# Kernel tuning notes

Hardware: AMD Instinct MI355X
Metric: run time of the kernel (lower is better)

Reference implementation:

```python
import jax, jax.numpy as jnp
import numpy as np

N_HEADS = 16


def setup_inputs() -> dict:
    key = jax.random.key(0)
    ks = jax.random.split(key, 9)
    B, S, D = 2, 2048, 1024
    s = 0.02
    return {
        "x": jax.random.normal(ks[0], (B, S, D), dtype=jnp.float32),
        "Wq": jax.random.normal(ks[1], (D, D), dtype=jnp.float32) * s,
        "bq": jax.random.normal(ks[2], (D,), dtype=jnp.float32) * s,
        "Wk": jax.random.normal(ks[3], (D, D), dtype=jnp.float32) * s,
        "bk": jax.random.normal(ks[4], (D,), dtype=jnp.float32) * s,
        "Wv": jax.random.normal(ks[5], (D, D), dtype=jnp.float32) * s,
        "bv": jax.random.normal(ks[6], (D,), dtype=jnp.float32) * s,
        "Wo": jax.random.normal(ks[7], (D, D), dtype=jnp.float32) * s,
        "bo": jax.random.normal(ks[8], (D,), dtype=jnp.float32) * s,
    }


def reference(x, Wq, bq, Wk, bk, Wv, bv, Wo, bo):
    B, S, D = x.shape
    H = N_HEADS
    hd = D // H
    # projections -> [B, H, S, hd]
    def heads(w, b):
        return (x @ w + b).reshape(B, S, H, hd).transpose(0, 2, 1, 3)
    Q, K, V = heads(Wq, bq), heads(Wk, bk), heads(Wv, bv)
    scores = jnp.einsum("bhqd,bhkd->bhqk", Q, K)
    causal = jnp.triu(jnp.ones((S, S), dtype=bool), k=1)  # True above diagonal
    scores = jnp.where(causal, -jnp.inf, scores)
    w = jax.nn.softmax(scores / jnp.sqrt(jnp.float32(hd)), axis=-1)
    ctx = jnp.einsum("bhqk,bhkd->bhqd", w, V).transpose(0, 2, 1, 3).reshape(B, S, D)
    return ctx @ Wo + bo
```

## Files before the change

kernel.cpp:

```cpp
#include <hip/hip_runtime.h>
#include <hip/hip_bf16.h>

typedef __attribute__((ext_vector_type(8))) short short8;
typedef __attribute__((ext_vector_type(4))) float floatx4;
typedef __attribute__((ext_vector_type(4))) int intx4;

#define D_MODEL 1024
#define SEQ     2048
#define NB      2
#define NH      16
#define HD      64
#define MROWS   4096
#define CZ      (0.125f * 1.44269504f)

__device__ __forceinline__ floatx4 mfma_bf16(short8 a, short8 b, floatx4 c) {
  return __builtin_amdgcn_mfma_f32_16x16x32_bf16(a, b, c, 0, 0, 0);
}

__device__ __forceinline__ void dma16(const __hip_bfloat16* g, __hip_bfloat16* l) {
  __builtin_amdgcn_global_load_lds(
      (const __attribute__((address_space(1))) void*)g,
      (__attribute__((address_space(3))) void*)l, 16, 0, 0);
}
#define WAIT_VM(n)  __asm__ __volatile__("s_waitcnt vmcnt(" #n ")" ::: "memory")
#define BARRIER()   __asm__ __volatile__("s_barrier" ::: "memory")

__device__ __forceinline__ int packbf(float a, float b) {
  union { __hip_bfloat16 h; unsigned short u; } x, y;
  x.h = __float2bfloat16(a); y.h = __float2bfloat16(b);
  return (int)(((unsigned)y.u << 16) | (unsigned)x.u);
}

__global__ void convert_x_kernel(const float* __restrict__ x, __hip_bfloat16* __restrict__ xb) {
  int i = (blockIdx.x * 256 + threadIdx.x) * 4;
  float4 v = *(const float4*)(x + i);
  __hip_bfloat16 tmp[4];
  tmp[0] = __float2bfloat16(v.x);
  tmp[1] = __float2bfloat16(v.y);
  tmp[2] = __float2bfloat16(v.z);
  tmp[3] = __float2bfloat16(v.w);
  *(ushort4*)(xb + i) = *(ushort4*)tmp;
}

__global__ void transpose_w_kernel(const float* __restrict__ W0, const float* __restrict__ W1,
                                   const float* __restrict__ W2, const float* __restrict__ W3,
                                   __hip_bfloat16* __restrict__ T0, __hip_bfloat16* __restrict__ T1,
                                   __hip_bfloat16* __restrict__ T2, __hip_bfloat16* __restrict__ T3) {
  const int z = blockIdx.z;
  const float* W = (z == 0) ? W0 : (z == 1) ? W1 : (z == 2) ? W2 : W3;
  __hip_bfloat16* Wt = (z == 0) ? T0 : (z == 1) ? T1 : (z == 2) ? T2 : T3;
  __shared__ float tile[32][33];
  int k0 = blockIdx.x * 32, n0 = blockIdx.y * 32;
  int tx = threadIdx.x, ty = threadIdx.y;
#pragma unroll
  for (int i = 0; i < 4; i++)
    tile[ty + 8 * i][tx] = W[(size_t)(k0 + ty + 8 * i) * D_MODEL + n0 + tx];
  __syncthreads();
#pragma unroll
  for (int i = 0; i < 4; i++)
    Wt[(size_t)(n0 + ty + 8 * i) * D_MODEL + k0 + tx] = __float2bfloat16(tile[tx][ty + 8 * i]);
}

template <int MODE>
__global__ __launch_bounds__(256) void gemm_kernel(
    const __hip_bfloat16* __restrict__ X,
    const __hip_bfloat16* __restrict__ Wt0, const __hip_bfloat16* __restrict__ Wt1,
    const __hip_bfloat16* __restrict__ Wt2,
    const float* __restrict__ b0, const float* __restrict__ b1, const float* __restrict__ b2,
    void* __restrict__ out0, void* __restrict__ out1, void* __restrict__ out2) {
  constexpr int MT = (MODE == 0) ? 128 : 64;
  constexpr int I = MT / 32;
  constexpr int NKT = D_MODEL / 32;

  const int z = blockIdx.y;
  const __hip_bfloat16* Wt = (z == 0) ? Wt0 : (z == 1) ? Wt1 : Wt2;
  const float* bias = (z == 0) ? b0 : (z == 1) ? b1 : b2;
  void* outp = (z == 0) ? out0 : (z == 1) ? out1 : out2;
  const float scale = (MODE == 0 && z == 0) ? CZ : 1.f;

  __shared__ __attribute__((aligned(16))) __hip_bfloat16 As[3][MT * 32];
  __shared__ __attribute__((aligned(16))) __hip_bfloat16 Bs[3][128 * 32];

  const int n0 = blockIdx.x * 128;
  const int m0 = blockIdx.z * MT;
  const int t = threadIdx.x;
  const int lane = t & 63, w = t >> 6;
  const int wm = (w >> 1) * (MT / 2), wn = (w & 1) * 64;
  const int lr = lane & 15;
  const int lq = lane >> 4;

  const __hip_bfloat16* Xp = X + (size_t)m0 * D_MODEL;
  const __hip_bfloat16* Wp = Wt + (size_t)n0 * D_MODEL;

  const int lrow = lane >> 2;
  const int skg = (lane & 3) << 3;
  const int srowA = ((MT == 128) ? (w << 5) : (w << 4)) + lrow;
  const int sbA0 = (((MT == 128) ? (w << 5) : (w << 4)) << 5);
  const int sbA1 = sbA0 + (16 << 5);
  const int srowB = (w << 5) + lrow;
  const int sbB0 = ((w << 5) << 5);
  const int sbB1 = sbB0 + (16 << 5);

#define STAGE_G(kt_, buf_)                                                              \
  {                                                                                     \
    const int kn_ = (kt_) * 32;                                                         \
    dma16(Xp + (size_t)srowA * D_MODEL + kn_ + skg, &As[buf_][sbA0]);                   \
    if (MT == 128) dma16(Xp + (size_t)(srowA + 16) * D_MODEL + kn_ + skg, &As[buf_][sbA1]); \
    dma16(Wp + (size_t)srowB * D_MODEL + kn_ + skg, &Bs[buf_][sbB0]);                   \
    dma16(Wp + (size_t)(srowB + 16) * D_MODEL + kn_ + skg, &Bs[buf_][sbB1]);            \
  }

  floatx4 acc[I][4];
#pragma unroll
  for (int i = 0; i < I; i++)
#pragma unroll
    for (int j = 0; j < 4; j++) acc[i][j] = (floatx4){0.f, 0.f, 0.f, 0.f};

  STAGE_G(0, 0);
  STAGE_G(1, 1);

  int cb = 0;
  for (int kt = 0; kt < NKT; kt++) {
    if (kt < NKT - 1) {
      if constexpr (MODE == 0) WAIT_VM(4);
      else                     WAIT_VM(3);
    } else {
      WAIT_VM(0);
    }
    BARRIER();
    if (kt + 2 < NKT) {
      const int nb = (cb == 0) ? 2 : cb - 1;
      STAGE_G(kt + 2, nb);
    }
    const __hip_bfloat16* Ac = As[cb];
    const __hip_bfloat16* Bc = Bs[cb];
    short8 af[I], bfr[4];
#pragma unroll
    for (int i = 0; i < I; i++) af[i] = *(const short8*)&Ac[(wm + i * 16 + lr) * 32 + lq * 8];
#pragma unroll
    for (int j = 0; j < 4; j++) bfr[j] = *(const short8*)&Bc[(wn + j * 16 + lr) * 32 + lq * 8];
#pragma unroll
    for (int i = 0; i < I; i++)
#pragma unroll
      for (int j = 0; j < 4; j++) acc[i][j] = mfma_bf16(af[i], bfr[j], acc[i][j]);
    cb = (cb == 2) ? 0 : cb + 1;
  }
#undef STAGE_G

#pragma unroll
  for (int j = 0; j < 4; j++) {
    const int n = n0 + wn + j * 16 + lr;
    const float bv = bias[n];
#pragma unroll
    for (int i = 0; i < I; i++) {
      const int mb = m0 + wm + i * 16 + lq * 4;
      if (MODE == 0) {
        __hip_bfloat16* O = (__hip_bfloat16*)outp;
        const int b = mb >> 11, s = mb & 2047;
        const int h = n >> 6, d = n & 63;
        if (z == 2) {
          ushort4 pk;
          __hip_bfloat16* pp = (__hip_bfloat16*)&pk;
#pragma unroll
          for (int r = 0; r < 4; r++) pp[r] = __float2bfloat16(acc[i][j][r] + bv);
          *(ushort4*)(O + (((size_t)(b * NH + h) * HD + d) * SEQ + s)) = pk;
        } else {
#pragma unroll
          for (int r = 0; r < 4; r++)
            O[(((size_t)(b * NH + h) * SEQ + (s + r)) * HD) + d] =
                __float2bfloat16((acc[i][j][r] + bv) * scale);
        }
      } else {
#pragma unroll
        for (int r = 0; r < 4; r++)
          ((float*)outp)[(size_t)(mb + r) * D_MODEL + n] = acc[i][j][r] + bv;
      }
    }
  }
}

__global__ __launch_bounds__(512, 4) void attn_kernel(
    const __hip_bfloat16* __restrict__ Q, const __hip_bfloat16* __restrict__ Kg,
    const __hip_bfloat16* __restrict__ Vt, __hip_bfloat16* __restrict__ ctx) {
  const int bh = blockIdx.x;
  const int b = bh >> 4, h = bh & 15;
  const int p = blockIdx.y;
  const int t = threadIdx.x, lane = t & 63, w = t >> 6;
  const int lr = lane & 15, lq = lane >> 4;
  const int wr = w & 3, wb = w >> 2;

  __shared__ __attribute__((aligned(16))) __hip_bfloat16 Ks[2][128 * 64];
  __shared__ __attribute__((aligned(16))) __hip_bfloat16 VTs[2][64 * 128];

  const __hip_bfloat16* Qb = Q + (size_t)bh * SEQ * HD;
  const __hip_bfloat16* Kb = Kg + (size_t)bh * SEQ * HD;
  const __hip_bfloat16* Vb = Vt + (size_t)bh * HD * SEQ;

  short8 qf[2][2];
#pragma unroll
  for (int ph = 0; ph < 2; ph++) {
    const int qt = ph ? 31 - p : p;
    const int rw = qt * 64 + wr * 16;
#pragma unroll
    for (int ks = 0; ks < 2; ks++)
      qf[ph][ks] = *(const short8*)(Qb + (size_t)(rw + lr) * HD + ks * 32 + lq * 8);
  }

  const int kr0 = (w << 4) + (lane >> 3);
  const int kg0 = (lane & 7) ^ (kr0 & 7);
  const int kr1 = kr0 + 8;
  const int kg1 = (lane & 7) ^ (kr1 & 7);
  const int kb0 = (w << 4) << 6;
  const int kb1 = ((w << 4) + 8) << 6;
  const int vr0 = (w << 3) + (lane >> 4);
  const int vg0 = (lane & 15) ^ (vr0 & 15);
  const int vr1 = vr0 + 4;
  const int vg1 = (lane & 15) ^ (vr1 & 15);
  const int vb0 = (w << 3) << 7;
  const int vb1 = ((w << 3) + 4) << 7;

  const int nktA = (p + 2) >> 1;
  const int TOT = 17;

#define STAGE(nn, nb)                                                           \
  {                                                                             \
    dma16(Kb + ((size_t)((nn) + kr0) << 6) + (kg0 << 3), &Ks[nb][kb0]);         \
    dma16(Kb + ((size_t)((nn) + kr1) << 6) + (kg1 << 3), &Ks[nb][kb1]);         \
    dma16(Vb + (size_t)vr0 * SEQ + (nn) + (vg0 << 3), &VTs[nb][vb0]);           \
    dma16(Vb + (size_t)vr1 * SEQ + (nn) + (vg1 << 3), &VTs[nb][vb1]);           \
  }

  STAGE(0, 0);
  int g = 0;

  const int idx0 = (lr + ((lq & 1) << 5)) << 2;
  const int idx1 = idx0 + 64;
  const bool hi = (lq >= 2);

  for (int ph = 0; ph < 2; ph++) {
    const int qt = ph ? 31 - p : p;
    const int nkt = (qt + 2) >> 1;
    const int rw = qt * 64 + wr * 16;
    const int q = rw + lr;

    floatx4 o[4];
#pragma unroll
    for (int dt = 0; dt < 4; dt++) o[dt] = (floatx4){0.f, 0.f, 0.f, 0.f};
    float ls = 0.f;

    for (int kt = 0; kt < nkt; kt++, g++) {
      WAIT_VM(0);
      BARRIER();
      if (g + 1 < TOT) {
        const int gn = g + 1;
        const int ktn = (gn < nktA) ? gn : gn - nktA;
        STAGE(ktn << 7, gn & 1);
      }
      const int n0 = (kt << 7) + (wb << 6);
      if (n0 <= rw + 15) {
        const __hip_bfloat16* Kc = Ks[g & 1];
        const __hip_bfloat16* Vc = VTs[g & 1];

        floatx4 s[4];
#pragma unroll
        for (int nt = 0; nt < 4; nt++) s[nt] = (floatx4){0.f, 0.f, 0.f, 0.f};
#pragma unroll
        for (int ks = 0; ks < 2; ks++) {
#pragma unroll
          for (int nt = 0; nt < 4; nt++) {
            const int row = (wb << 6) + (nt << 4) + lr;
            short8 kf = *(const short8*)&Kc[(row << 6) + ((((ks << 2) + lq) ^ (row & 7)) << 3)];
            s[nt] = mfma_bf16(kf, qf[ph][ks], s[nt]);
          }
        }

        int pkA[4], pkB[4];
        if (n0 + 63 > rw) {
#pragma unroll
          for (int nt = 0; nt < 4; nt++) {
            const int kbase = n0 + (nt << 4) + (lq << 2);
            float pe[4];
#pragma unroll
            for (int r = 0; r < 4; r++) {
              pe[r] = (kbase + r <= q) ? exp2f(s[nt][r]) : 0.f;
              ls += pe[r];
            }
            pkA[nt] = packbf(pe[0], pe[1]);
            pkB[nt] = packbf(pe[2], pe[3]);
          }
        } else {
#pragma unroll
          for (int nt = 0; nt < 4; nt++) {
            float pe[4];
#pragma unroll
            for (int r = 0; r < 4; r++) {
              pe[r] = exp2f(s[nt][r]);
              ls += pe[r];
            }
            pkA[nt] = packbf(pe[0], pe[1]);
            pkB[nt] = packbf(pe[2], pe[3]);
          }
        }

#pragma unroll
        for (int ks = 0; ks < 2; ks++) {
          const int t0 = 2 * ks, t1 = 2 * ks + 1;
          int c0a = __builtin_amdgcn_ds_bpermute(idx0, pkA[t0]);
          int c0b = __builtin_amdgcn_ds_bpermute(idx0, pkA[t1]);
          int c1a = __builtin_amdgcn_ds_bpermute(idx0, pkB[t0]);
          int c1b = __builtin_amdgcn_ds_bpermute(idx0, pkB[t1]);
          int c2a = __builtin_amdgcn_ds_bpermute(idx1, pkA[t0]);
          int c2b = __builtin_amdgcn_ds_bpermute(idx1, pkA[t1]);
          int c3a = __builtin_amdgcn_ds_bpermute(idx1, pkB[t0]);
          int c3b = __builtin_amdgcn_ds_bpermute(idx1, pkB[t1]);
          intx4 bi;
          bi[0] = hi ? c0b : c0a;
          bi[1] = hi ? c1b : c1a;
          bi[2] = hi ? c2b : c2a;
          bi[3] = hi ? c3b : c3a;
          short8 pf = __builtin_bit_cast(short8, bi);
#pragma unroll
          for (int dt = 0; dt < 4; dt++) {
            const int row = (dt << 4) + lr;
            const int gv = (wb << 3) + (ks << 2) + lq;
            short8 vf = *(const short8*)&Vc[(row << 7) + ((gv ^ (row & 15)) << 3)];
            o[dt] = mfma_bf16(vf, pf, o[dt]);
          }
        }
      }
    }

    const int fb = (g - 1) & 1;
    BARRIER();
    {
      float* od = (float*)&Ks[fb][0];
      float* ld = (float*)&VTs[fb][0];
      const int base = (wr << 10) + (lane << 4);
      if (wb == 1) {
#pragma unroll
        for (int dt = 0; dt < 4; dt++) *(floatx4*)&od[base + (dt << 2)] = o[dt];
        ld[(wr << 6) + lane] = ls;
      }
      BARRIER();
      if (wb == 0) {
#pragma unroll
        for (int dt = 0; dt < 4; dt++) o[dt] += *(const floatx4*)&od[base + (dt << 2)];
        ls += ld[(wr << 6) + lane];
        ls += __shfl_xor(ls, 16);
        ls += __shfl_xor(ls, 32);
        const float inv = 1.f / ls;
        __hip_bfloat16* cp = ctx + (size_t)b * SEQ * D_MODEL + h * HD + (size_t)q * D_MODEL;
#pragma unroll
        for (int dt = 0; dt < 4; dt++) {
          ushort4 pk;
          __hip_bfloat16* pp = (__hip_bfloat16*)&pk;
#pragma unroll
          for (int r = 0; r < 4; r++) pp[r] = __float2bfloat16(o[dt][r] * inv);
          *(ushort4*)(cp + (dt << 4) + (lq << 2)) = pk;
        }
      }
    }
  }
#undef STAGE
}

extern "C" void kernel_launch(void* const* d_in, const int* in_sizes, int n_in,
                              void* d_out, int out_size, void* d_ws, size_t ws_size,
                              hipStream_t stream) {
  const float* x  = (const float*)d_in[0];
  const float* Wq = (const float*)d_in[1];
  const float* bq = (const float*)d_in[2];
  const float* Wk = (const float*)d_in[3];
  const float* bk = (const float*)d_in[4];
  const float* Wv = (const float*)d_in[5];
  const float* bv = (const float*)d_in[6];
  const float* Wo = (const float*)d_in[7];
  const float* bo = (const float*)d_in[8];

  char* ws = (char*)d_ws;
  const size_t MB = 1u << 20;
  __hip_bfloat16* xb  = (__hip_bfloat16*)(ws + 0 * MB);
  __hip_bfloat16* wtq = (__hip_bfloat16*)(ws + 8 * MB);
  __hip_bfloat16* wtk = (__hip_bfloat16*)(ws + 10 * MB);
  __hip_bfloat16* wtv = (__hip_bfloat16*)(ws + 12 * MB);
  __hip_bfloat16* wto = (__hip_bfloat16*)(ws + 14 * MB);
  __hip_bfloat16* qb  = (__hip_bfloat16*)(ws + 16 * MB);
  __hip_bfloat16* kb  = (__hip_bfloat16*)(ws + 24 * MB);
  __hip_bfloat16* vt  = (__hip_bfloat16*)(ws + 32 * MB);
  __hip_bfloat16* ctx = xb;

  convert_x_kernel<<<4096, 256, 0, stream>>>(x, xb);
  transpose_w_kernel<<<dim3(32, 32, 4), dim3(32, 8), 0, stream>>>(Wq, Wk, Wv, Wo,
                                                                  wtq, wtk, wtv, wto);
  gemm_kernel<0><<<dim3(8, 3, 32), 256, 0, stream>>>(xb, wtq, wtk, wtv, bq, bk, bv,
                                                     (void*)qb, (void*)kb, (void*)vt);
  attn_kernel<<<dim3(32, 16), 512, 0, stream>>>(qb, kb, vt, ctx);
  gemm_kernel<1><<<dim3(8, 1, 64), 256, 0, stream>>>(ctx, wto, wto, wto, bo, bo, bo,
                                                     d_out, d_out, d_out);
}
```

Measured before the change: 199.8 us.

## Halve attention block to 4 waves with two row tiles each; fuse prep kernels

The attention kernel drops from 8 to 4 waves per block. Each wave now computes two 16-row query tiles, so every K and V fragment read from LDS is reused across two MFMAs. Masked scores are set to a large negative before exp, bf16 packing uses a perm-based round instead of the library conversion, and the cross-wave reduction gets its own LDS buffers. The x conversion and weight transpose launches are merged into one prep kernel to save a launch. In exchange, register pressure rises and there are fewer waves per CU to hide latency.

```diff
diff --git a/kernel.cpp b/kernel.cpp
--- a/kernel.cpp
+++ b/kernel.cpp
@@ -24,29 +24,35 @@
 }
 #define WAIT_VM(n)  __asm__ __volatile__("s_waitcnt vmcnt(" #n ")" ::: "memory")
 #define BARRIER()   __asm__ __volatile__("s_barrier" ::: "memory")
-
-__device__ __forceinline__ int packbf(float a, float b) {
-  union { __hip_bfloat16 h; unsigned short u; } x, y;
-  x.h = __float2bfloat16(a); y.h = __float2bfloat16(b);
-  return (int)(((unsigned)y.u << 16) | (unsigned)x.u);
-}
-
-__global__ void convert_x_kernel(const float* __restrict__ x, __hip_bfloat16* __restrict__ xb) {
-  int i = (blockIdx.x * 256 + threadIdx.x) * 4;
-  float4 v = *(const float4*)(x + i);
-  __hip_bfloat16 tmp[4];
-  tmp[0] = __float2bfloat16(v.x);
-  tmp[1] = __float2bfloat16(v.y);
-  tmp[2] = __float2bfloat16(v.z);
-  tmp[3] = __float2bfloat16(v.w);
-  *(ushort4*)(xb + i) = *(ushort4*)tmp;
-}
-
-__global__ void transpose_w_kernel(const float* __restrict__ W0, const float* __restrict__ W1,
-                                   const float* __restrict__ W2, const float* __restrict__ W3,
-                                   __hip_bfloat16* __restrict__ T0, __hip_bfloat16* __restrict__ T1,
-                                   __hip_bfloat16* __restrict__ T2, __hip_bfloat16* __restrict__ T3) {
+#define WAIT_LGKM() __asm__ __volatile__("s_waitcnt lgkmcnt(0)" ::: "memory")
+
+__device__ __forceinline__ int pack2bf(float a, float b) {
+  unsigned ua = __builtin_bit_cast(unsigned, a) + 0x8000u;
+  unsigned ub = __builtin_bit_cast(unsigned, b) + 0x8000u;
+  return (int)__builtin_amdgcn_perm(ub, ua, 0x07060302u);
+}
+
+__global__ void prep_kernel(const float* __restrict__ x, __hip_bfloat16* __restrict__ xb,
+                            const float* __restrict__ W0, const float* __restrict__ W1,
+                            const float* __restrict__ W2, const float* __restrict__ W3,
+                            __hip_bfloat16* __restrict__ T0, __hip_bfloat16* __restrict__ T1,
+                            __hip_bfloat16* __restrict__ T2, __hip_bfloat16* __restrict__ T3) {
   const int z = blockIdx.z;
+  if (z == 4) {
+    const int tid = threadIdx.y * 32 + threadIdx.x;
+    const int base = ((blockIdx.y * 32 + blockIdx.x) * 256 + tid) * 16;
+#pragma unroll
+    for (int c = 0; c < 4; c++) {
+      float4 v = *(const float4*)(x + base + c * 4);
+      __hip_bfloat16 tmp[4];
+      tmp[0] = __float2bfloat16(v.x);
+      tmp[1] = __float2bfloat16(v.y);
+      tmp[2] = __float2bfloat16(v.z);
+      tmp[3] = __float2bfloat16(v.w);
+      *(ushort4*)(xb + base + c * 4) = *(ushort4*)tmp;
+    }
+    return;
+  }
   const float* W = (z == 0) ? W0 : (z == 1) ? W1 : (z == 2) ? W2 : W3;
   __hip_bfloat16* Wt = (z == 0) ? T0 : (z == 1) ? T1 : (z == 2) ? T2 : T3;
   __shared__ float tile[32][33];
@@ -179,7 +185,7 @@
   }
 }
 
-__global__ __launch_bounds__(512, 4) void attn_kernel(
+__global__ __launch_bounds__(256, 2) void attn_kernel(
     const __hip_bfloat16* __restrict__ Q, const __hip_bfloat16* __restrict__ Kg,
     const __hip_bfloat16* __restrict__ Vt, __hip_bfloat16* __restrict__ ctx) {
   const int bh = blockIdx.x;
@@ -187,48 +193,51 @@
   const int p = blockIdx.y;
   const int t = threadIdx.x, lane = t & 63, w = t >> 6;
   const int lr = lane & 15, lq = lane >> 4;
-  const int wr = w & 3, wb = w >> 2;
+  const int wr = w & 1, wb = w >> 1;
 
   __shared__ __attribute__((aligned(16))) __hip_bfloat16 Ks[2][128 * 64];
   __shared__ __attribute__((aligned(16))) __hip_bfloat16 VTs[2][64 * 128];
+  __shared__ __attribute__((aligned(16))) float dumpO[2048];
+  __shared__ float dumpL[256];
 
   const __hip_bfloat16* Qb = Q + (size_t)bh * SEQ * HD;
   const __hip_bfloat16* Kb = Kg + (size_t)bh * SEQ * HD;
   const __hip_bfloat16* Vb = Vt + (size_t)bh * HD * SEQ;
 
-  short8 qf[2][2];
+  short8 qf[2][2][2];
 #pragma unroll
   for (int ph = 0; ph < 2; ph++) {
     const int qt = ph ? 31 - p : p;
-    const int rw = qt * 64 + wr * 16;
-#pragma unroll
-    for (int ks = 0; ks < 2; ks++)
-      qf[ph][ks] = *(const short8*)(Qb + (size_t)(rw + lr) * HD + ks * 32 + lq * 8);
-  }
-
-  const int kr0 = (w << 4) + (lane >> 3);
-  const int kg0 = (lane & 7) ^ (kr0 & 7);
-  const int kr1 = kr0 + 8;
-  const int kg1 = (lane & 7) ^ (kr1 & 7);
-  const int kb0 = (w << 4) << 6;
-  const int kb1 = ((w << 4) + 8) << 6;
-  const int vr0 = (w << 3) + (lane >> 4);
-  const int vg0 = (lane & 15) ^ (vr0 & 15);
-  const int vr1 = vr0 + 4;
-  const int vg1 = (lane & 15) ^ (vr1 & 15);
-  const int vb0 = (w << 3) << 7;
-  const int vb1 = ((w << 3) + 4) << 7;
+#pragma unroll
+    for (int rt = 0; rt < 2; rt++)
+#pragma unroll
+      for (int ks = 0; ks < 2; ks++)
+        qf[ph][rt][ks] = *(const short8*)(Qb + (size_t)(qt * 64 + wr * 32 + rt * 16 + lr) * HD +
+                                          ks * 32 + lq * 8);
+  }
+
+  const int krow = (w << 5) + (lane >> 3);
+  const int ksl = lane & 7;
+  const int vrow = (w << 4) + (lane >> 4);
+  const int vsl = lane & 15;
+
+#define STAGE(tb, nb)                                                                     \
+  {                                                                                       \
+    _Pragma("unroll") for (int i = 0; i < 4; i++) {                                       \
+      const int r_ = krow + i * 8;                                                        \
+      dma16(Kb + ((size_t)((tb) + r_) << 6) + ((ksl ^ (r_ & 7)) << 3),                    \
+            &Ks[nb][((w << 5) + i * 8) << 6]);                                            \
+    }                                                                                     \
+    _Pragma("unroll") for (int i = 0; i < 4; i++) {                                       \
+      const int r_ = vrow + i * 4;                                                        \
+      dma16(Vb + (size_t)r_ * SEQ + (tb) + ((vsl ^ (r_ & 15)) << 3),                      \
+            &VTs[nb][((w << 4) + i * 4) << 7]);                                           \
+    }                                                                                     \
+  }
 
   const int nktA = (p + 2) >> 1;
   const int TOT = 17;
-
-#define STAGE(nn, nb)                                                           \
-  {                                                                             \
-    dma16(Kb + ((size_t)((nn) + kr0) << 6) + (kg0 << 3), &Ks[nb][kb0]);         \
-    dma16(Kb + ((size_t)((nn) + kr1) << 6) + (kg1 << 3), &Ks[nb][kb1]);         \
-    dma16(Vb + (size_t)vr0 * SEQ + (nn) + (vg0 << 3), &VTs[nb][vb0]);           \
-    dma16(Vb + (size_t)vr1 * SEQ + (nn) + (vg1 << 3), &VTs[nb][vb1]);           \
-  }
+#define KTN(gs) (((gs) < nktA) ? (gs) : (gs)-nktA)
 
   STAGE(0, 0);
   int g = 0;
@@ -237,131 +246,163 @@
   const int idx1 = idx0 + 64;
   const bool hi = (lq >= 2);
 
+  const int kfb0 = (lr << 6) + ((lq ^ (lr & 7)) << 3);
+  const int kfb1 = (lr << 6) + (((4 + lq) ^ (lr & 7)) << 3);
+  const int vfb0 = (lr << 7) + ((((wb << 3) + lq) ^ lr) << 3);
+  const int vfb1 = (lr << 7) + ((((wb << 3) + 4 + lq) ^ lr) << 3);
+  const int kwoff = wb << 12;
+
   for (int ph = 0; ph < 2; ph++) {
     const int qt = ph ? 31 - p : p;
     const int nkt = (qt + 2) >> 1;
-    const int rw = qt * 64 + wr * 16;
-    const int q = rw + lr;
-
-    floatx4 o[4];
-#pragma unroll
-    for (int dt = 0; dt < 4; dt++) o[dt] = (floatx4){0.f, 0.f, 0.f, 0.f};
-    float ls = 0.f;
+    const int qbase = qt * 64 + wr * 32;
+    const int qmaxw = qbase + 31;
+
+    floatx4 o[2][4];
+#pragma unroll
+    for (int rt = 0; rt < 2; rt++)
+#pragma unroll
+      for (int dt = 0; dt < 4; dt++) o[rt][dt] = (floatx4){0.f, 0.f, 0.f, 0.f};
+    float ls[2] = {0.f, 0.f};
 
     for (int kt = 0; kt < nkt; kt++, g++) {
       WAIT_VM(0);
       BARRIER();
-      if (g + 1 < TOT) {
-        const int gn = g + 1;
-        const int ktn = (gn < nktA) ? gn : gn - nktA;
-        STAGE(ktn << 7, gn & 1);
-      }
-      const int n0 = (kt << 7) + (wb << 6);
-      if (n0 <= rw + 15) {
-        const __hip_bfloat16* Kc = Ks[g & 1];
-        const __hip_bfloat16* Vc = VTs[g & 1];
-
-        floatx4 s[4];
-#pragma unroll
-        for (int nt = 0; nt < 4; nt++) s[nt] = (floatx4){0.f, 0.f, 0.f, 0.f};
-#pragma unroll
-        for (int ks = 0; ks < 2; ks++) {
+      if (g + 1 < TOT) STAGE(KTN(g + 1) << 7, (g + 1) & 1);
+
+      const int n0w = (kt << 7) + (wb << 6);
+      if (n0w <= qmaxw) {
+        const int cbuf = g & 1;
+        const __hip_bfloat16* Kc = &Ks[cbuf][kwoff];
+        const __hip_bfloat16* Vc = VTs[cbuf];
+
+        short8 kf[2][4];
+#pragma unroll
+        for (int nt = 0; nt < 4; nt++) {
+          kf[0][nt] = *(const short8*)&Kc[(nt << 10) + kfb0];
+          kf[1][nt] = *(const short8*)&Kc[(nt << 10) + kfb1];
+        }
+        floatx4 s[2][4];
+#pragma unroll
+        for (int rt = 0; rt < 2; rt++)
+#pragma unroll
+          for (int nt = 0; nt < 4; nt++) s[rt][nt] = (floatx4){0.f, 0.f, 0.f, 0.f};
+#pragma unroll
+        for (int ks = 0; ks < 2; ks++)
 #pragma unroll
           for (int nt = 0; nt < 4; nt++) {
-            const int row = (wb << 6) + (nt << 4) + lr;
-            short8 kf = *(const short8*)&Kc[(row << 6) + ((((ks << 2) + lq) ^ (row & 7)) << 3)];
-            s[nt] = mfma_bf16(kf, qf[ph][ks], s[nt]);
+            s[0][nt] = mfma_bf16(kf[ks][nt], qf[ph][0][ks], s[0][nt]);
+            s[1][nt] = mfma_bf16(kf[ks][nt], qf[ph][1][ks], s[1][nt]);
+          }
+
+        int pkA[2][4], pkB[2][4];
+        const bool need_mask = (n0w + 63 > qbase);
+#pragma unroll
+        for (int rt = 0; rt < 2; rt++) {
+          const int q = qbase + rt * 16 + lr;
+#pragma unroll
+          for (int nt = 0; nt < 4; nt++) {
+            const int kbase = n0w + (nt << 4) + (lq << 2);
+            float x0 = s[rt][nt][0], x1 = s[rt][nt][1], x2 = s[rt][nt][2], x3 = s[rt][nt][3];
+            if (need_mask) {
+              x0 = (kbase + 0 <= q) ? x0 : -1e30f;
+              x1 = (kbase + 1 <= q) ? x1 : -1e30f;
+              x2 = (kbase + 2 <= q) ? x2 : -1e30f;
+              x3 = (kbase + 3 <= q) ? x3 : -1e30f;
+            }
+            const float p0 = __builtin_amdgcn_exp2f(x0);
+            const float p1 = __builtin_amdgcn_exp2f(x1);
+            const float p2 = __builtin_amdgcn_exp2f(x2);
+            const float p3 = __builtin_amdgcn_exp2f(x3);
+            ls[rt] += (p0 + p1) + (p2 + p3);
+            pkA[rt][nt] = pack2bf(p0, p1);
+            pkB[rt][nt] = pack2bf(p2, p3);
           }
         }
 
-        int pkA[4], pkB[4];
-        if (n0 + 63 > rw) {
-#pragma unroll
-          for (int nt = 0; nt < 4; nt++) {
-            const int kbase = n0 + (nt << 4) + (lq << 2);
-            float pe[4];
-#pragma unroll
-            for (int r = 0; r < 4; r++) {
-              pe[r] = (kbase + r <= q) ? exp2f(s[nt][r]) : 0.f;
-              ls += pe[r];
-            }
-            pkA[nt] = packbf(pe[0], pe[1]);
-            pkB[nt] = packbf(pe[2], pe[3]);
+#pragma unroll
+        for (int ks = 0; ks < 2; ks++) {
+          short8 pf[2];
+#pragma unroll
+          for (int rt = 0; rt < 2; rt++) {
+            const int t0 = 2 * ks, t1 = 2 * ks + 1;
+            int c0a = __builtin_amdgcn_ds_bpermute(idx0, pkA[rt][t0]);
+            int c0b = __builtin_amdgcn_ds_bpermute(idx0, pkA[rt][t1]);
+            int c1a = __builtin_amdgcn_ds_bpermute(idx0, pkB[rt][t0]);
+            int c1b = __builtin_amdgcn_ds_bpermute(idx0, pkB[rt][t1]);
+            int c2a = __builtin_amdgcn_ds_bpermute(idx1, pkA[rt][t0]);
+            int c2b = __builtin_amdgcn_ds_bpermute(idx1, pkA[rt][t1]);
+            int c3a = __builtin_amdgcn_ds_bpermute(idx1, pkB[rt][t0]);
+            int c3b = __builtin_amdgcn_ds_bpermute(idx1, pkB[rt][t1]);
+            intx4 bi;
+            bi[0] = hi ? c0b : c0a;
+            bi[1] = hi ? c1b : c1a;
+            bi[2] = hi ? c2b : c2a;
+            bi[3] = hi ? c3b : c3a;
+            pf[rt] = __builtin_bit_cast(short8, bi);
           }
-        } else {
-#pragma unroll
-          for (int nt = 0; nt < 4; nt++) {
-            float pe[4];
-#pragma unroll
-            for (int r = 0; r < 4; r++) {
-              pe[r] = exp2f(s[nt][r]);
-              ls += pe[r];
-            }
-            pkA[nt] = packbf(pe[0], pe[1]);
-            pkB[nt] = packbf(pe[2], pe[3]);
-          }
-        }
-
-#pragma unroll
-        for (int ks = 0; ks < 2; ks++) {
-          const int t0 = 2 * ks, t1 = 2 * ks + 1;
-          int c0a = __builtin_amdgcn_ds_bpermute(idx0, pkA[t0]);
-          int c0b = __builtin_amdgcn_ds_bpermute(idx0, pkA[t1]);
-          int c1a = __builtin_amdgcn_ds_bpermute(idx0, pkB[t0]);
-          int c1b = __builtin_amdgcn_ds_bpermute(idx0, pkB[t1]);
-          int c2a = __builtin_amdgcn_ds_bpermute(idx1, pkA[t0]);
-          int c2b = __builtin_amdgcn_ds_bpermute(idx1, pkA[t1]);
-          int c3a = __builtin_amdgcn_ds_bpermute(idx1, pkB[t0]);
-          int c3b = __builtin_amdgcn_ds_bpermute(idx1, pkB[t1]);
-          intx4 bi;
-          bi[0] = hi ? c0b : c0a;
-          bi[1] = hi ? c1b : c1a;
-          bi[2] = hi ? c2b : c2a;
-          bi[3] = hi ? c3b : c3a;
-          short8 pf = __builtin_bit_cast(short8, bi);
+          const int vfb = ks ? vfb1 : vfb0;
 #pragma unroll
           for (int dt = 0; dt < 4; dt++) {
-            const int row = (dt << 4) + lr;
-            const int gv = (wb << 3) + (ks << 2) + lq;
-            short8 vf = *(const short8*)&Vc[(row << 7) + ((gv ^ (row & 15)) << 3)];
-            o[dt] = mfma_bf16(vf, pf, o[dt]);
+            short8 vf = *(const short8*)&Vc[(dt << 11) + vfb];
+            o[0][dt] = mfma_bf16(vf, pf[0], o[0][dt]);
+            o[1][dt] = mfma_bf16(vf, pf[1], o[1][dt]);
           }
         }
       }
     }
 
-    const int fb = (g - 1) & 1;
+    const int dbase = (wr << 10) + (lane << 4);
     BARRIER();
-    {
-      float* od = (float*)&Ks[fb][0];
-      float* ld = (float*)&VTs[fb][0];
-      const int base = (wr << 10) + (lane << 4);
-      if (wb == 1) {
-#pragma unroll
-        for (int dt = 0; dt < 4; dt++) *(floatx4*)&od[base + (dt << 2)] = o[dt];
-        ld[(wr << 6) + lane] = ls;
+    if (wb == 1) {
+#pragma unroll
+      for (int dt = 0; dt < 4; dt++) *(floatx4*)&dumpO[dbase + (dt << 2)] = o[0][dt];
+      dumpL[(wr << 7) + (lane << 1)] = ls[0];
+      dumpL[(wr << 7) + (lane << 1) + 1] = ls[1];
+      WAIT_LGKM();
+    }
+    BARRIER();
+    if (wb == 0) {
+#pragma unroll
+      for (int dt = 0; dt < 4; dt++) o[0][dt] += *(const floatx4*)&dumpO[dbase + (dt << 2)];
+      ls[0] += dumpL[(wr << 7) + (lane << 1)];
+      ls[1] += dumpL[(wr << 7) + (lane << 1) + 1];
+    }
+    BARRIER();
+    if (wb == 1) {
+#pragma unroll
+      for (int dt = 0; dt < 4; dt++) *(floatx4*)&dumpO[dbase + (dt << 2)] = o[1][dt];
+      WAIT_LGKM();
+    }
+    BARRIER();
+    if (wb == 0) {
+#pragma unroll
+      for (int dt = 0; dt < 4; dt++) o[1][dt] += *(const floatx4*)&dumpO[dbase + (dt << 2)];
+      float inv[2];
+#pragma unroll
+      for (int rt = 0; rt < 2; rt++) {
+        float v = ls[rt];
+        v += __shfl_xor(v, 16);
+        v += __shfl_xor(v, 32);
+        inv[rt] = 1.f / v;
       }
-      BARRIER();
-      if (wb == 0) {
-#pragma unroll
-        for (int dt = 0; dt < 4; dt++) o[dt] += *(const floatx4*)&od[base + (dt << 2)];
-        ls += ld[(wr << 6) + lane];
-        ls += __shfl_xor(ls, 16);
-        ls += __shfl_xor(ls, 32);
-        const float inv = 1.f / ls;
-        __hip_bfloat16* cp = ctx + (size_t)b * SEQ * D_MODEL + h * HD + (size_t)q * D_MODEL;
+#pragma unroll
+      for (int rt = 0; rt < 2; rt++) {
+        const int row = qbase + rt * 16 + lr;
+        __hip_bfloat16* cp = ctx + (size_t)b * SEQ * D_MODEL + (size_t)row * D_MODEL + h * HD;
 #pragma unroll
         for (int dt = 0; dt < 4; dt++) {
           ushort4 pk;
           __hip_bfloat16* pp = (__hip_bfloat16*)&pk;
 #pragma unroll
-          for (int r = 0; r < 4; r++) pp[r] = __float2bfloat16(o[dt][r] * inv);
+          for (int r = 0; r < 4; r++) pp[r] = __float2bfloat16(o[rt][dt][r] * inv[rt]);
           *(ushort4*)(cp + (dt << 4) + (lq << 2)) = pk;
         }
       }
     }
   }
 #undef STAGE
+#undef KTN
 }
 
 extern "C" void kernel_launch(void* const* d_in, const int* in_sizes, int n_in,
@@ -389,12 +430,11 @@
   __hip_bfloat16* vt  = (__hip_bfloat16*)(ws + 32 * MB);
   __hip_bfloat16* ctx = xb;
 
-  convert_x_kernel<<<4096, 256, 0, stream>>>(x, xb);
-  transpose_w_kernel<<<dim3(32, 32, 4), dim3(32, 8), 0, stream>>>(Wq, Wk, Wv, Wo,
-                                                                  wtq, wtk, wtv, wto);
+  prep_kernel<<<dim3(32, 32, 5), dim3(32, 8), 0, stream>>>(x, xb, Wq, Wk, Wv, Wo,
+                                                           wtq, wtk, wtv, wto);
   gemm_kernel<0><<<dim3(8, 3, 32), 256, 0, stream>>>(xb, wtq, wtk, wtv, bq, bk, bv,
                                                      (void*)qb, (void*)kb, (void*)vt);
-  attn_kernel<<<dim3(32, 16), 512, 0, stream>>>(qb, kb, vt, ctx);
+  attn_kernel<<<dim3(32, 16), 256, 0, stream>>>(qb, kb, vt, ctx);
   gemm_kernel<1><<<dim3(8, 1, 64), 256, 0, stream>>>(ctx, wto, wto, wto, bo, bo, bo,
                                                      d_out, d_out, d_out);
 }
```

Result: faster. 194.6 us (-2.6%).
